# Kernel optimization log

Hardware: AMD Instinct MI355X
Metric: run time of the kernel (lower is better)

## Reference

```python
import jax, jax.numpy as jnp
import numpy as np

D_K = 64
N_HEADS = 12
LN_EPS = 1e-5


def layer_norm(x, eps=LN_EPS):
    # nn.LayerNorm(768) is created fresh each forward -> weight=1, bias=0
    mu = jnp.mean(x, axis=-1, keepdims=True)
    var = jnp.mean(jnp.square(x - mu), axis=-1, keepdims=True)
    return (x - mu) * jax.lax.rsqrt(var + eps)


def setup_inputs() -> dict:
    key = jax.random.key(0)
    ks = jax.random.split(key, 7)
    B, S, D = 2, 2048, 768
    scale = 1.0 / np.sqrt(D)
    return {
        "input_Q": jax.random.normal(ks[0], (B, S, D), jnp.float32),
        "input_K": jax.random.normal(ks[1], (B, S, D), jnp.float32),
        "input_V": jax.random.normal(ks[2], (B, S, D), jnp.float32),
        "Wq": jax.random.normal(ks[3], (D, D), jnp.float32) * scale,
        "Wk": jax.random.normal(ks[4], (D, D), jnp.float32) * scale,
        "Wv": jax.random.normal(ks[5], (D, D), jnp.float32) * scale,
        "Wo": jax.random.normal(ks[6], (D, D), jnp.float32) * scale,
    }


def reference(input_Q, input_K, input_V, Wq, Wk, Wv, Wo):
    B, Sq, D = input_Q.shape
    Sk = input_K.shape[1]
    H, dk = N_HEADS, D_K
    residual = input_Q
    # projections: [B,S,D] @ [D, H*dk] -> [B,H,S,dk]
    Q = (input_Q @ Wq).reshape(B, Sq, H, dk).transpose(0, 2, 1, 3)
    K = (input_K @ Wk).reshape(B, Sk, H, dk).transpose(0, 2, 1, 3)
    V = (input_V @ Wv).reshape(B, Sk, H, dk).transpose(0, 2, 1, 3)
    # attention scores [B,H,Sq,Sk]
    att = jnp.einsum("bhqd,bhkd->bhqk", Q, K) / np.sqrt(dk).astype(np.float32)
    att = jax.nn.softmax(att, axis=-1)
    ctx = jnp.einsum("bhqk,bhkd->bhqd", att, V)  # [B,H,Sq,dk]
    ctx = ctx.transpose(0, 2, 1, 3).reshape(B, Sq, H * dk)
    out = ctx @ Wo
    return layer_norm(out + residual)
```

## Files before the change

### kernel.cpp

```cpp
#include <hip/hip_runtime.h>
#include <hip/hip_bf16.h>
#include <stdint.h>

#define S_LEN 2048
#define D_MODEL 768
#define NH 12
#define DK 64
#define BATCH 2
#define M_TOT (BATCH * S_LEN)

typedef __attribute__((ext_vector_type(8))) short short8;
typedef __attribute__((ext_vector_type(4))) float f32x4;
typedef __attribute__((ext_vector_type(16))) float f32x16;

__device__ inline short f2bf(float f) {
  union { float f; uint32_t u; } v; v.f = f;
  uint32_t r = v.u + 0x7fffu + ((v.u >> 16) & 1u);
  return (short)(r >> 16);
}

__device__ inline f32x4 mfma16(short8 a, short8 b, f32x4 c) {
  return __builtin_amdgcn_mfma_f32_16x16x32_bf16(a, b, c, 0, 0, 0);
}
__device__ inline f32x16 mfma32(short8 a, short8 b, f32x16 c) {
  return __builtin_amdgcn_mfma_f32_32x32x16_bf16(a, b, c, 0, 0, 0);
}

__device__ inline void gl16(const void* g, void* l) {
  __builtin_amdgcn_global_load_lds(
      (const __attribute__((address_space(1))) unsigned*)g,
      (__attribute__((address_space(3))) unsigned*)l, 16, 0, 0);
}

__device__ inline unsigned cvtpk(float lo, float hi) {
  unsigned r;
  asm("v_cvt_pk_bf16_f32 %0, %1, %2" : "=v"(r) : "v"(lo), "v"(hi));
  return r;
}
__device__ inline void plswap(unsigned& a, unsigned& b) {
  asm("v_permlane32_swap_b32 %0, %1" : "+v"(a), "+v"(b));
}

__global__ __launch_bounds__(256) void transpose_w_kernel(
    const float* __restrict__ Wq, const float* __restrict__ Wk,
    const float* __restrict__ Wv, const float* __restrict__ Wo,
    short* __restrict__ WT) {
  int z = blockIdx.z;
  const float* W = z == 0 ? Wq : (z == 1 ? Wk : (z == 2 ? Wv : Wo));
  short* O = WT + (size_t)z * D_MODEL * D_MODEL;
  __shared__ float t[32][33];
  int x = threadIdx.x, y = threadIdx.y;
  int nb = blockIdx.x * 32, kb = blockIdx.y * 32;
#pragma unroll
  for (int j = 0; j < 4; ++j)
    t[y + 8 * j][x] = W[(kb + y + 8 * j) * D_MODEL + nb + x];
  __syncthreads();
#pragma unroll
  for (int j = 0; j < 4; ++j)
    O[(nb + y + 8 * j) * D_MODEL + kb + x] = f2bf(t[x][y + 8 * j]);
}

__global__ __launch_bounds__(256) void cast_x_kernel(
    const float* __restrict__ Xq, const float* __restrict__ Xk,
    const float* __restrict__ Xv, short* __restrict__ Xb) {
  int z = blockIdx.y;
  const float* X = z == 0 ? Xq : (z == 1 ? Xk : Xv);
  short* O = Xb + (size_t)z * M_TOT * D_MODEL;
  size_t i = ((size_t)blockIdx.x * 256 + threadIdx.x) * 8;
  float4 f0 = *(const float4*)(X + i);
  float4 f1 = *(const float4*)(X + i + 4);
  short8 v;
  v[0] = f2bf(f0.x); v[1] = f2bf(f0.y); v[2] = f2bf(f0.z); v[3] = f2bf(f0.w);
  v[4] = f2bf(f1.x); v[5] = f2bf(f1.y); v[6] = f2bf(f1.z); v[7] = f2bf(f1.w);
  *(short8*)(O + i) = v;
}

__global__ __launch_bounds__(256) void proj_kernel(
    const short* __restrict__ Xb, const short* __restrict__ WTall,
    short* __restrict__ Qo, short* __restrict__ Ko, short* __restrict__ Vo) {
  int bid = blockIdx.x;
  int wk = (bid & 7) * 72 + (bid >> 3);
  int which = wk / 192;
  int rem = wk % 192;
  int mt = rem / 6, nt = rem % 6;
  int mbase = mt * 128, nbase = nt * 128;
  const short* X = Xb + (size_t)which * M_TOT * D_MODEL;
  const short* WT = WTall + (size_t)which * D_MODEL * D_MODEL;

  __shared__ short As[128][32];
  __shared__ short Bs[128][32];
  int tid = threadIdx.x;
  int wv = tid >> 6, lane = tid & 63, r = lane & 15, g = lane >> 4;
  int wm = (wv & 1) * 64, wn = (wv >> 1) * 64;
  int srow = (lane >> 2), scol = (lane & 3) * 8;

  f32x4 acc[4][4] = {};
  for (int kk = 0; kk < D_MODEL; kk += 32) {
#pragma unroll
    for (int j = 0; j < 2; ++j) {
      int row = wv * 32 + j * 16;
      gl16(X + (size_t)(mbase + row + srow) * D_MODEL + kk + scol, &As[row][0]);
      gl16(WT + (size_t)(nbase + row + srow) * D_MODEL + kk + scol, &Bs[row][0]);
    }
    __syncthreads();
    short8 a[4], b[4];
#pragma unroll
    for (int i = 0; i < 4; ++i) {
      a[i] = *(short8*)&As[wm + i * 16 + r][g * 8];
      b[i] = *(short8*)&Bs[wn + i * 16 + r][g * 8];
    }
#pragma unroll
    for (int i = 0; i < 4; ++i)
#pragma unroll
      for (int j = 0; j < 4; ++j)
        acc[i][j] = mfma16(a[i], b[j], acc[i][j]);
    __syncthreads();
  }
#pragma unroll
  for (int i = 0; i < 4; ++i)
#pragma unroll
    for (int j = 0; j < 4; ++j)
#pragma unroll
      for (int reg = 0; reg < 4; ++reg) {
        int m = mbase + wm + i * 16 + g * 4 + reg;
        int n = nbase + wn + j * 16 + r;
        int b_ = m >> 11, s = m & 2047, h = n >> 6, d = n & 63;
        if (which == 0) {
          short v = f2bf(acc[i][j][reg] * 0.18033688f);
          Qo[(((size_t)b_ * NH + h) * S_LEN + s) * DK + d] = v;
        } else if (which == 1) {
          short v = f2bf(acc[i][j][reg]);
          Ko[(((size_t)b_ * NH + h) * S_LEN + s) * DK + (d ^ ((s & 7) << 3))] = v;
        } else {
          short v = f2bf(acc[i][j][reg]);
          Vo[(((size_t)b_ * NH + h) * DK + d) * S_LEN + (s ^ ((d & 7) << 3))] = v;
        }
      }
}

__global__ __launch_bounds__(128) void attn_kernel(
    const short* __restrict__ Qg, const short* __restrict__ Kg,
    const short* __restrict__ Vt, short* __restrict__ ctx) {
  __shared__ char K_lds[2][8192];
  __shared__ char V_lds[2][8192];
  int bh = blockIdx.y;
  int b = bh / NH, h = bh % NH;
  int tid = threadIdx.x;
  int w = tid >> 6, lane = tid & 63;
  int c32 = lane & 31, hi = lane >> 5;
  int qbase = blockIdx.x * 64 + w * 32;
  const short* qp = Qg + (size_t)bh * S_LEN * DK;
  const char* kp = (const char*)(Kg + (size_t)bh * S_LEN * DK);
  const char* vp = (const char*)(Vt + (size_t)bh * DK * S_LEN);

  short8 qf[4];
#pragma unroll
  for (int kk = 0; kk < 4; ++kk)
    qf[kk] = *(const short8*)(qp + (size_t)(qbase + c32) * DK + kk * 16 + hi * 8);

#define STAGE(buf, kc)                                                          \
  {                                                                             \
    _Pragma("unroll") for (int j = 0; j < 4; ++j) {                             \
      int p = w * 4 + j;                                                        \
      gl16(kp + (size_t)(kc)*128 + p * 1024 + lane * 16, &K_lds[buf][p * 1024]);\
    }                                                                           \
    _Pragma("unroll") for (int j = 0; j < 4; ++j) {                             \
      int p = w * 4 + j;                                                        \
      int row = p * 8 + (lane >> 3);                                            \
      gl16(vp + (size_t)row * 4096 + (kc)*2 + (lane & 7) * 16,                  \
           &V_lds[buf][p * 1024]);                                              \
    }                                                                           \
  }

  STAGE(0, 0);

  f32x16 o0 = {}, o1 = {};
  float m_run = -30000.f, l_run = 0.f;
  int cur = 0;

  for (int t = 0; t < S_LEN / 64; ++t) {
    if (t < S_LEN / 64 - 1) {
      STAGE(cur ^ 1, (t + 1) * 64);
      asm volatile("s_waitcnt vmcnt(8)" ::: "memory");
    } else {
      asm volatile("s_waitcnt vmcnt(0)" ::: "memory");
    }
    __builtin_amdgcn_s_barrier();

    const char* kb = K_lds[cur];
    const char* vb = V_lds[cur];

    f32x16 st0 = {}, st1 = {};
#pragma unroll
    for (int kk = 0; kk < 4; ++kk) {
      int cb = kk * 32 + hi * 16;
      short8 k0 = *(const short8*)(kb + c32 * 128 + (cb ^ ((c32 & 7) << 4)));
      short8 k1 = *(const short8*)(kb + (32 + c32) * 128 + (cb ^ ((c32 & 7) << 4)));
      st0 = mfma32(k0, qf[kk], st0);
      st1 = mfma32(k1, qf[kk], st1);
    }

    float cm = -30000.f;
#pragma unroll
    for (int i = 0; i < 16; ++i) cm = fmaxf(cm, fmaxf(st0[i], st1[i]));
    cm = fmaxf(cm, __shfl_xor(cm, 32));
    if (!__all(cm <= m_run + 8.0f)) {
      float m_new = fmaxf(m_run, cm);
      float al = __builtin_amdgcn_exp2f(m_run - m_new);
      l_run *= al;
      m_run = m_new;
#pragma unroll
      for (int r = 0; r < 16; ++r) {
        int ql = (r & 3) + 8 * (r >> 2) + 4 * hi;
        float ar = __shfl(al, ql);
        o0[r] *= ar;
        o1[r] *= ar;
      }
    }
    float csum = 0.f;
#pragma unroll
    for (int i = 0; i < 16; ++i) {
      st0[i] = __builtin_amdgcn_exp2f(st0[i] - m_run);
      st1[i] = __builtin_amdgcn_exp2f(st1[i] - m_run);
      csum += st0[i] + st1[i];
    }
    csum += __shfl_xor(csum, 32);
    l_run += csum;

#pragma unroll
    for (int ks = 0; ks < 4; ++ks) {
      f32x16 P = (ks < 2) ? st0 : st1;
      int s8 = (ks & 1) * 8;
      unsigned A = cvtpk(P[s8 + 0], P[s8 + 1]);
      unsigned Bx = cvtpk(P[s8 + 4], P[s8 + 5]);
      unsigned C = cvtpk(P[s8 + 2], P[s8 + 3]);
      unsigned Dx = cvtpk(P[s8 + 6], P[s8 + 7]);
      plswap(A, Bx);
      plswap(C, Dx);
      union { unsigned u[4]; short8 s; } pu;
      pu.u[0] = A; pu.u[1] = C; pu.u[2] = Bx; pu.u[3] = Dx;
      int cb = ks * 32 + hi * 16;
      short8 v0 = *(const short8*)(vb + c32 * 128 + (cb ^ ((c32 & 7) << 4)));
      short8 v1 = *(const short8*)(vb + (32 + c32) * 128 + (cb ^ ((c32 & 7) << 4)));
      o0 = mfma32(pu.s, v0, o0);
      o1 = mfma32(pu.s, v1, o1);
    }

    __builtin_amdgcn_s_barrier();
    cur ^= 1;
  }

  size_t rowbase = (size_t)b * S_LEN + qbase;
#pragma unroll
  for (int r = 0; r < 16; ++r) {
    int ql = (r & 3) + 8 * (r >> 2) + 4 * hi;
    float linv = 1.0f / __shfl(l_run, ql);
    short* cp = ctx + (rowbase + ql) * D_MODEL + h * DK;
    cp[c32] = f2bf(o0[r] * linv);
    cp[32 + c32] = f2bf(o1[r] * linv);
  }
#undef STAGE
}

__global__ __launch_bounds__(256) void gemm_out_kernel(
    const short* __restrict__ ctx, const short* __restrict__ WoT,
    const float* __restrict__ resid, float* __restrict__ Y) {
  int bid = blockIdx.x;
  int wk = (bid & 7) * 24 + (bid >> 3);
  int mt = wk / 6, nt = wk % 6;
  int mbase = mt * 128, nbase = nt * 128;

  __shared__ short As[128][32];
  __shared__ short Bs[128][32];
  int tid = threadIdx.x;
  int wv = tid >> 6, lane = tid & 63, r = lane & 15, g = lane >> 4;
  int wm = (wv & 1) * 64, wn = (wv >> 1) * 64;
  int srow = (lane >> 2), scol = (lane & 3) * 8;

  f32x4 acc[4][4] = {};
  for (int kk = 0; kk < D_MODEL; kk += 32) {
#pragma unroll
    for (int j = 0; j < 2; ++j) {
      int row = wv * 32 + j * 16;
      gl16(ctx + (size_t)(mbase + row + srow) * D_MODEL + kk + scol, &As[row][0]);
      gl16(WoT + (size_t)(nbase + row + srow) * D_MODEL + kk + scol, &Bs[row][0]);
    }
    __syncthreads();
    short8 a[4], b[4];
#pragma unroll
    for (int i = 0; i < 4; ++i) {
      a[i] = *(short8*)&As[wm + i * 16 + r][g * 8];
      b[i] = *(short8*)&Bs[wn + i * 16 + r][g * 8];
    }
#pragma unroll
    for (int i = 0; i < 4; ++i)
#pragma unroll
      for (int j = 0; j < 4; ++j)
        acc[i][j] = mfma16(a[i], b[j], acc[i][j]);
    __syncthreads();
  }
#pragma unroll
  for (int i = 0; i < 4; ++i)
#pragma unroll
    for (int j = 0; j < 4; ++j)
#pragma unroll
      for (int reg = 0; reg < 4; ++reg) {
        int m = mbase + wm + i * 16 + g * 4 + reg;
        int n = nbase + wn + j * 16 + r;
        Y[(size_t)m * D_MODEL + n] = acc[i][j][reg] + resid[(size_t)m * D_MODEL + n];
      }
}

__global__ __launch_bounds__(256) void ln_kernel(const float* __restrict__ Y,
                                                 float* __restrict__ out) {
  int row = blockIdx.x * 4 + (threadIdx.x >> 6);
  int l = threadIdx.x & 63;
  const float* yp = Y + (size_t)row * D_MODEL;
  float v[12];
  float s = 0.f, q = 0.f;
#pragma unroll
  for (int c = 0; c < 12; ++c) {
    v[c] = yp[c * 64 + l];
    s += v[c];
    q += v[c] * v[c];
  }
#pragma unroll
  for (int d = 1; d < 64; d <<= 1) {
    s += __shfl_xor(s, d);
    q += __shfl_xor(q, d);
  }
  float mu = s * (1.0f / 768.0f);
  float var = q * (1.0f / 768.0f) - mu * mu;
  float rstd = rsqrtf(var + 1e-5f);
  float* op = out + (size_t)row * D_MODEL;
#pragma unroll
  for (int c = 0; c < 12; ++c)
    op[c * 64 + l] = (v[c] - mu) * rstd;
}

extern "C" void kernel_launch(void* const* d_in, const int* in_sizes, int n_in,
                              void* d_out, int out_size, void* d_ws, size_t ws_size,
                              hipStream_t stream) {
  const float* xq = (const float*)d_in[0];
  const float* xk = (const float*)d_in[1];
  const float* xv = (const float*)d_in[2];
  const float* Wq = (const float*)d_in[3];
  const float* Wk = (const float*)d_in[4];
  const float* Wv = (const float*)d_in[5];
  const float* Wo = (const float*)d_in[6];
  float* out = (float*)d_out;

  char* ws = (char*)d_ws;
  const size_t WSZ = (size_t)D_MODEL * D_MODEL;
  const size_t QSZ = (size_t)M_TOT * D_MODEL;
  short* WT = (short*)ws;
  short* Xb = WT + 4 * WSZ;
  short* Qb = Xb + 3 * QSZ;
  short* Kb = Qb + QSZ;
  short* Vb = Kb + QSZ;
  short* Cx = Vb + QSZ;
  float* Yf = (float*)Xb;

  transpose_w_kernel<<<dim3(24, 24, 4), dim3(32, 8), 0, stream>>>(Wq, Wk, Wv, Wo, WT);
  cast_x_kernel<<<dim3(1536, 3), 256, 0, stream>>>(xq, xk, xv, Xb);
  proj_kernel<<<576, 256, 0, stream>>>(Xb, WT, Qb, Kb, Vb);
  attn_kernel<<<dim3(32, 24), 128, 0, stream>>>(Qb, Kb, Vb, Cx);
  gemm_out_kernel<<<192, 256, 0, stream>>>(Cx, WT + 3 * WSZ, xq, Yf);
  ln_kernel<<<1024, 256, 0, stream>>>(Yf, out);
}
```

Before: 226.0 us.

## Split attention over two key halves and merge partials in a separate kernel

Attention now runs with a grid z-dimension of 2, each block handling half the key sequence. Each block writes normalized bf16 partial outputs plus running max and sum to scratch space. A new merge kernel combines the two halves with log-sum-exp weights and writes the context in the original layout. The aim is more blocks in flight to fill the GPU, at the cost of an extra kernel launch, extra global traffic, and bf16 rounding of the intermediate partials.

```diff
diff --git a/kernel.cpp b/kernel.cpp
--- a/kernel.cpp
+++ b/kernel.cpp
@@ -39,6 +39,12 @@
 }
 __device__ inline void plswap(unsigned& a, unsigned& b) {
   asm("v_permlane32_swap_b32 %0, %1" : "+v"(a), "+v"(b));
+}
+__device__ inline float lo16(uint32_t u) {
+  union { uint32_t u; float f; } x; x.u = u << 16; return x.f;
+}
+__device__ inline float hi16(uint32_t u) {
+  union { uint32_t u; float f; } x; x.u = u & 0xffff0000u; return x.f;
 }
 
 __global__ __launch_bounds__(256) void transpose_w_kernel(
@@ -140,15 +146,17 @@
 
 __global__ __launch_bounds__(128) void attn_kernel(
     const short* __restrict__ Qg, const short* __restrict__ Kg,
-    const short* __restrict__ Vt, short* __restrict__ ctx) {
+    const short* __restrict__ Vt, short* __restrict__ oP,
+    float* __restrict__ mlP) {
   __shared__ char K_lds[2][8192];
   __shared__ char V_lds[2][8192];
   int bh = blockIdx.y;
-  int b = bh / NH, h = bh % NH;
+  int split = blockIdx.z;
   int tid = threadIdx.x;
   int w = tid >> 6, lane = tid & 63;
   int c32 = lane & 31, hi = lane >> 5;
   int qbase = blockIdx.x * 64 + w * 32;
+  int kc0 = split * (S_LEN / 2);
   const short* qp = Qg + (size_t)bh * S_LEN * DK;
   const char* kp = (const char*)(Kg + (size_t)bh * S_LEN * DK);
   const char* vp = (const char*)(Vt + (size_t)bh * DK * S_LEN);
@@ -172,15 +180,16 @@
     }                                                                           \
   }
 
-  STAGE(0, 0);
+  STAGE(0, kc0);
 
   f32x16 o0 = {}, o1 = {};
   float m_run = -30000.f, l_run = 0.f;
   int cur = 0;
-
-  for (int t = 0; t < S_LEN / 64; ++t) {
-    if (t < S_LEN / 64 - 1) {
-      STAGE(cur ^ 1, (t + 1) * 64);
+  const int NT = (S_LEN / 2) / 64;
+
+  for (int t = 0; t < NT; ++t) {
+    if (t < NT - 1) {
+      STAGE(cur ^ 1, kc0 + (t + 1) * 64);
       asm volatile("s_waitcnt vmcnt(8)" ::: "memory");
     } else {
       asm volatile("s_waitcnt vmcnt(0)" ::: "memory");
@@ -250,16 +259,43 @@
     cur ^= 1;
   }
 
-  size_t rowbase = (size_t)b * S_LEN + qbase;
+  size_t pbase = ((size_t)split * 24 + bh) * S_LEN;
 #pragma unroll
   for (int r = 0; r < 16; ++r) {
     int ql = (r & 3) + 8 * (r >> 2) + 4 * hi;
     float linv = 1.0f / __shfl(l_run, ql);
-    short* cp = ctx + (rowbase + ql) * D_MODEL + h * DK;
-    cp[c32] = f2bf(o0[r] * linv);
-    cp[32 + c32] = f2bf(o1[r] * linv);
+    short* op = oP + (pbase + qbase + ql) * DK;
+    op[c32] = f2bf(o0[r] * linv);
+    op[32 + c32] = f2bf(o1[r] * linv);
+  }
+  if (hi == 0) {
+    float* mlp = mlP + (pbase + qbase + c32) * 2;
+    mlp[0] = m_run;
+    mlp[1] = l_run;
   }
 #undef STAGE
+}
+
+__global__ __launch_bounds__(256) void merge_kernel(
+    const short* __restrict__ oP, const float* __restrict__ mlP,
+    short* __restrict__ Cx) {
+  int t = blockIdx.x * 256 + threadIdx.x;
+  int q = t >> 5, dp = (t & 31) * 2;
+  const int NQ = 24 * S_LEN;
+  float2 ml0 = *(const float2*)(mlP + (size_t)q * 2);
+  float2 ml1 = *(const float2*)(mlP + ((size_t)NQ + q) * 2);
+  float m = fmaxf(ml0.x, ml1.x);
+  float a0 = ml0.y * __builtin_amdgcn_exp2f(ml0.x - m);
+  float a1 = ml1.y * __builtin_amdgcn_exp2f(ml1.x - m);
+  float inv = 1.0f / (a0 + a1);
+  float w0 = a0 * inv, w1 = a1 * inv;
+  uint32_t a = *(const uint32_t*)(oP + (size_t)q * DK + dp);
+  uint32_t b2 = *(const uint32_t*)(oP + ((size_t)NQ + q) * DK + dp);
+  float v0 = lo16(a) * w0 + lo16(b2) * w1;
+  float v1 = hi16(a) * w0 + hi16(b2) * w1;
+  int bh = q >> 11, sr = q & 2047, b = bh / NH, h = bh % NH;
+  uint32_t outw = (uint32_t)(uint16_t)f2bf(v0) | ((uint32_t)(uint16_t)f2bf(v1) << 16);
+  *(uint32_t*)(Cx + ((size_t)(b * S_LEN + sr)) * D_MODEL + h * DK + dp) = outw;
 }
 
 __global__ __launch_bounds__(256) void gemm_out_kernel(
@@ -359,12 +395,15 @@
   short* Kb = Qb + QSZ;
   short* Vb = Kb + QSZ;
   short* Cx = Vb + QSZ;
+  short* oP = Xb;
+  float* mlP = (float*)(Xb + (size_t)2 * 24 * S_LEN * DK);
   float* Yf = (float*)Xb;
 
   transpose_w_kernel<<<dim3(24, 24, 4), dim3(32, 8), 0, stream>>>(Wq, Wk, Wv, Wo, WT);
   cast_x_kernel<<<dim3(1536, 3), 256, 0, stream>>>(xq, xk, xv, Xb);
   proj_kernel<<<576, 256, 0, stream>>>(Xb, WT, Qb, Kb, Vb);
-  attn_kernel<<<dim3(32, 24), 128, 0, stream>>>(Qb, Kb, Vb, Cx);
+  attn_kernel<<<dim3(32, 24, 2), 128, 0, stream>>>(Qb, Kb, Vb, oP, mlP);
+  merge_kernel<<<6144, 256, 0, stream>>>(oP, mlP, Cx);
   gemm_out_kernel<<<192, 256, 0, stream>>>(Cx, WT + 3 * WSZ, xq, Yf);
   ln_kernel<<<1024, 256, 0, stream>>>(Yf, out);
 }
```

Result: slower. 233.3 us (+3.2%).
